# Kernel tuning notes

Hardware: AMD Instinct MI355X
Metric: run time of the kernel (lower is better)

## Reference

```python
import jax, jax.numpy as jnp
import numpy as np

NUM_NODES = 256
IN_FEAT = 64
HIDDEN = 512
N_CLASSES = 2
BATCH = 256


def setup_inputs() -> dict:
    key = jax.random.key(0)
    ks = jax.random.split(key, 10)
    return {
        "z": jax.random.normal(ks[0], (BATCH, 1, NUM_NODES, NUM_NODES), dtype=jnp.float32),
        "node_emb": jax.random.normal(ks[1], (NUM_NODES, IN_FEAT), dtype=jnp.float32),
        "w1": jax.random.normal(ks[2], (IN_FEAT, HIDDEN), dtype=jnp.float32) * (1.0 / np.sqrt(IN_FEAT)),
        "b1": jnp.zeros((HIDDEN,), dtype=jnp.float32),
        "w2": jax.random.normal(ks[3], (HIDDEN, HIDDEN), dtype=jnp.float32) * (1.0 / np.sqrt(HIDDEN)),
        "b2": jnp.zeros((HIDDEN,), dtype=jnp.float32),
        "w3": jax.random.normal(ks[4], (HIDDEN, HIDDEN), dtype=jnp.float32) * (1.0 / np.sqrt(HIDDEN)),
        "b3": jnp.zeros((HIDDEN,), dtype=jnp.float32),
        "fcw": jax.random.normal(ks[5], (HIDDEN, N_CLASSES), dtype=jnp.float32) * (1.0 / np.sqrt(HIDDEN)),
        "fcb": jnp.zeros((N_CLASSES,), dtype=jnp.float32),
    }


def reference(z, node_emb, w1, b1, w2, b2, w3, b3, fcw, fcb):
    # z: (B, 1, N, N) latent interpreted as weighted adjacency
    z_sq = jnp.squeeze(z, axis=1)                         # (B, N, N)
    A = jax.nn.sigmoid(z_sq)
    A = (A + jnp.swapaxes(A, 1, 2)) * 0.5                  # symmetrize
    A_hat = A + jnp.eye(A.shape[-1], dtype=A.dtype)[None]  # add self loops
    D_hat = jnp.sum(A_hat, axis=2) + 1e-6                  # (B, N) degrees
    d_inv_sqrt = D_hat ** -0.5
    # norm_A = D^{-1/2} A_hat D^{-1/2} via row/col scaling (same math as diag bmm)
    norm_A = A_hat * d_inv_sqrt[:, :, None] * d_inv_sqrt[:, None, :]

    X = jnp.broadcast_to(node_emb[None], (z.shape[0],) + node_emb.shape)  # (B, N, F)
    H1 = jax.nn.relu(jnp.einsum('bij,bjh->bih', norm_A, X @ w1 + b1))
    H2 = jax.nn.relu(jnp.einsum('bij,bjh->bih', norm_A, H1 @ w2 + b2))
    H3 = jax.nn.relu(jnp.einsum('bij,bjh->bih', norm_A, H2 @ w3 + b3))
    graph_emb = jnp.mean(H3, axis=1)                       # (B, H)
    logits = graph_emb @ fcw + fcb                         # (B, n_classes)
    return logits
```

## Files before the change

kernel.cpp:

```cpp
#include <hip/hip_runtime.h>
#include <stdint.h>

#define B_ 256
#define N_ 256
#define F_ 64
#define H_ 512

typedef _Float16 f16;
typedef _Float16 f16x8 __attribute__((ext_vector_type(8)));
typedef _Float16 f16x4 __attribute__((ext_vector_type(4)));
typedef float    f32x4 __attribute__((ext_vector_type(4)));

__device__ __forceinline__ float sigmoidf_(float x) {
    return 1.0f / (1.0f + __expf(-x));
}

__global__ __launch_bounds__(256) void k_pre(const float* __restrict__ z,
                                             const float* __restrict__ ne,
                                             const float* __restrict__ w1,
                                             const float* __restrict__ b1,
                                             const float* __restrict__ w2,
                                             const float* __restrict__ w3,
                                             f16* __restrict__ S,
                                             float* __restrict__ R,
                                             float* __restrict__ Cpart,
                                             f16* __restrict__ XW1t,
                                             f16* __restrict__ w2t,
                                             f16* __restrict__ w3t) {
    int bid = blockIdx.x;
    int tid = threadIdx.x;
    if (bid < 2048) {
        int b = bid >> 3, c = bid & 7;
        int lane = tid & 63, w = tid >> 6;
        float colacc[4] = {0.f, 0.f, 0.f, 0.f};
        for (int r = 0; r < 8; r++) {
            int i = c * 32 + w * 8 + r;
            size_t base = ((size_t)(b * N_ + i)) * N_;
            float4 v = *(const float4*)(z + base + lane * 4);
            float s0 = sigmoidf_(v.x), s1 = sigmoidf_(v.y),
                  s2 = sigmoidf_(v.z), s3 = sigmoidf_(v.w);
            f16x4 sv = { (f16)s0, (f16)s1, (f16)s2, (f16)s3 };
            *(f16x4*)(S + base + lane * 4) = sv;
            colacc[0] += s0; colacc[1] += s1; colacc[2] += s2; colacc[3] += s3;
            float rs = s0 + s1 + s2 + s3;
            for (int off = 32; off; off >>= 1) rs += __shfl_down(rs, off, 64);
            if (lane == 0) R[b * N_ + i] = rs;
        }
        __shared__ float cbuf[4][N_];
        #pragma unroll
        for (int k = 0; k < 4; k++) cbuf[w][lane * 4 + k] = colacc[k];
        __syncthreads();
        float s4 = cbuf[0][tid] + cbuf[1][tid] + cbuf[2][tid] + cbuf[3][tid];
        Cpart[((size_t)c * B_ + b) * N_ + tid] = s4;
    } else if (bid < 2560) {
        int h = bid - 2048, node = tid;
        float s = b1[h];
        #pragma unroll 8
        for (int k = 0; k < F_; k++) s += ne[node * F_ + k] * w1[k * H_ + h];
        XW1t[h * N_ + node] = (f16)s;
    } else {
        int idx4 = bid - 2560;
        int which = idx4 >> 10;
        const float* src = which ? w3 : w2;
        f16* dst = which ? w3t : w2t;
        int idx = (idx4 & 1023) * 256 + tid;
        int k = idx >> 9, n = idx & 511;
        dst[n * H_ + k] = (f16)src[k * H_ + n];
    }
}

__global__ __launch_bounds__(256) void k_norma3(const f16* __restrict__ S,
                                                const float* __restrict__ R,
                                                const float* __restrict__ Cpart,
                                                f16* __restrict__ nA) {
    __shared__ f16 T0[128 * 129];
    __shared__ f16 T1[128 * 129];
    __shared__ float Dv[N_];
    int b = blockIdx.y, t = blockIdx.x;
    int tid = threadIdx.x;
    const f16* Sb = S + (size_t)b * N_ * N_;
    f16* Ab = nA + (size_t)b * N_ * N_;

    float cs = 0.f;
    #pragma unroll
    for (int c = 0; c < 8; c++) cs += Cpart[((size_t)c * B_ + b) * N_ + tid];
    Dv[tid] = rsqrtf(1.0f + 1e-6f + 0.5f * (R[b * N_ + tid] + cs));

    auto stage = [&](const f16* src, f16* dst) {
        #pragma unroll
        for (int it = 0; it < 8; it++) {
            int u = it * 256 + tid;
            int r = u >> 4, c8 = (u & 15) * 8;
            *(f16x8*)&dst[r * 129 + c8] = *(const f16x8*)&src[(size_t)r * N_ + c8];
        }
    };
    if (t == 0)      stage(Sb, T0);
    else if (t == 1) stage(Sb + 128 * N_ + 128, T0);
    else           { stage(Sb + 128, T0); stage(Sb + (size_t)128 * N_, T1); }
    __syncthreads();

    auto emit = [&](const f16* Dir, const f16* Mir, int i0, int j0) {
        #pragma unroll
        for (int it = 0; it < 8; it++) {
            int il = it * 16 + (tid >> 4), jl8 = (tid & 15) * 8;
            float di = Dv[i0 + il];
            f16x8 d = *(const f16x8*)&Dir[il * 129 + jl8];
            f16x8 o;
            #pragma unroll
            for (int k = 0; k < 8; k++) {
                float v = 0.5f * ((float)d[k] + (float)Mir[(jl8 + k) * 129 + il]);
                if (i0 + il == j0 + jl8 + k) v += 1.0f;
                o[k] = (f16)(v * di * Dv[j0 + jl8 + k]);
            }
            *(f16x8*)&Ab[(size_t)(i0 + il) * N_ + j0 + jl8] = o;
        }
    };
    if (t == 0)      emit(T0, T0, 0, 0);
    else if (t == 1) emit(T0, T0, 128, 128);
    else           { emit(T0, T1, 0, 128); emit(T1, T0, 128, 0); }
}

template <int KDIM, int MODE>
__global__ __launch_bounds__(256, 4) void k_gemm(const f16* __restrict__ A, long aBatch,
                                                 const f16* __restrict__ Bt, long bBatch,
                                                 f16* __restrict__ Out,
                                                 const float* __restrict__ bias,
                                                 float* __restrict__ gp) {
    __shared__ f16 As[128 * 64];
    __shared__ f16 Bs[128 * 64];
    const int tid  = threadIdx.x;
    const int lane = tid & 63, wave = tid >> 6;
    const int wm = wave >> 1, wn = wave & 1;

    const int lin = blockIdx.x;
    const int xcd = lin & 7, q = lin >> 3;
    const int n_t = q & 3, p = q >> 2;
    const int grp = xcd * 64 + p;
    const int b   = grp >> 1, m_t = grp & 1;
    const int m0 = m_t * 128, n0 = n_t * 128;

    const f16* Ab = A + (size_t)b * aBatch;
    const f16* Bb = Bt + (size_t)b * bBatch;

    f32x4 acc[4][4];
    #pragma unroll
    for (int i = 0; i < 4; i++)
        #pragma unroll
        for (int j = 0; j < 4; j++)
            #pragma unroll
            for (int r = 0; r < 4; r++) acc[i][j][r] = 0.0f;

    const int lr = lane >> 3;
    const int kc = (lane & 7) ^ lr;

    const int ln15 = lane & 15;

    constexpr int NS = KDIM / 64;
    const int srot = ((q >> 5) + q) & (NS - 1);

    for (int si = 0; si < NS; si++) {
        const int kk = ((si + srot) & (NS - 1)) * 64;
        #pragma unroll
        for (int c = 0; c < 4; c++) {
            int chunk = wave * 4 + c;
            int row = chunk * 8 + lr;
            __builtin_amdgcn_global_load_lds(
                (__attribute__((address_space(1))) void*)(Ab + (size_t)(m0 + row) * KDIM + kk + kc * 8),
                (__attribute__((address_space(3))) void*)(&As[chunk * 512]), 16, 0, 0);
            __builtin_amdgcn_global_load_lds(
                (__attribute__((address_space(1))) void*)(Bb + (size_t)(n0 + row) * KDIM + kk + kc * 8),
                (__attribute__((address_space(3))) void*)(&Bs[chunk * 512]), 16, 0, 0);
        }
        __syncthreads();

        #pragma unroll
        for (int ks = 0; ks < 2; ks++) {
            const int rkc = ks * 4 + (lane >> 4);
            f16x8 aF[4];
            #pragma unroll
            for (int t = 0; t < 4; t++) {
                int ra = wm * 64 + t * 16 + ln15;
                aF[t] = *(const f16x8*)&As[(ra * 8 + (rkc ^ (ra & 7))) * 8];
            }
            #pragma unroll
            for (int h2 = 0; h2 < 2; h2++) {
                f16x8 bF[2];
                #pragma unroll
                for (int t = 0; t < 2; t++) {
                    int rb = wn * 64 + (h2 * 2 + t) * 16 + ln15;
                    bF[t] = *(const f16x8*)&Bs[(rb * 8 + (rkc ^ (rb & 7))) * 8];
                }
                #pragma unroll
                for (int mt = 0; mt < 4; mt++)
                    #pragma unroll
                    for (int t = 0; t < 2; t++)
                        acc[mt][h2 * 2 + t] = __builtin_amdgcn_mfma_f32_16x16x32_f16(aF[mt], bF[t], acc[mt][h2 * 2 + t], 0, 0, 0);
            }
        }
        __syncthreads();
    }

    const int quad = lane >> 4;
    if (MODE == 0) {
        f16* Ob = Out + (size_t)b * (N_ * H_);
        #pragma unroll
        for (int mt = 0; mt < 4; mt++) {
            int node = m0 + wm * 64 + mt * 16 + quad * 4;
            #pragma unroll
            for (int nt = 0; nt < 4; nt++) {
                int h = n0 + wn * 64 + nt * 16 + ln15;
                #pragma unroll
                for (int rr = 0; rr < 4; rr++) {
                    float v = acc[mt][nt][rr];
                    v = v > 0.f ? v : 0.f;
                    Ob[(size_t)(node + rr) * H_ + h] = (f16)v;
                }
            }
        }
    } else if (MODE == 1) {
        f16* Ob = Out + (size_t)b * (H_ * N_);
        #pragma unroll
        for (int nt = 0; nt < 4; nt++) {
            int n = n0 + wn * 64 + nt * 16 + ln15;
            float bv = bias[n];
            #pragma unroll
            for (int mt = 0; mt < 4; mt++) {
                int node = m0 + wm * 64 + mt * 16 + quad * 4;
                f16x4 v;
                #pragma unroll
                for (int rr = 0; rr < 4; rr++) v[rr] = (f16)(acc[mt][nt][rr] + bv);
                *(f16x4*)&Ob[(size_t)n * N_ + node] = v;
            }
        }
    } else {
        float part[4];
        #pragma unroll
        for (int nt = 0; nt < 4; nt++) {
            float partial = 0.f;
            #pragma unroll
            for (int mt = 0; mt < 4; mt++)
                #pragma unroll
                for (int rr = 0; rr < 4; rr++) {
                    float v = acc[mt][nt][rr];
                    partial += (v > 0.f ? v : 0.f);
                }
            partial += __shfl_down(partial, 32, 64);
            partial += __shfl_down(partial, 16, 64);
            part[nt] = partial;
        }
        __syncthreads();
        float* red = (float*)&As[0];
        if (quad == 0) {
            #pragma unroll
            for (int nt = 0; nt < 4; nt++)
                red[wave * 64 + nt * 16 + ln15] = part[nt];
        }
        __syncthreads();
        if (tid < 128) {
            int wnl = tid >> 6, hl = tid & 63;
            float v = red[wnl * 64 + hl] + red[(wnl + 2) * 64 + hl];
            gp[((size_t)m_t * B_ + b) * H_ + n0 + wnl * 64 + hl] = v;
        }
    }
}

__global__ __launch_bounds__(256) void k_logits(const float* __restrict__ gp,
                                                const float* __restrict__ fcw,
                                                const float* __restrict__ fcb,
                                                float* __restrict__ out) {
    int b = blockIdx.x, tid = threadIdx.x;
    const float* g0p = gp + (size_t)b * H_;
    const float* g1p = gp + (size_t)(B_ + b) * H_;
    float g0 = g0p[tid] + g1p[tid];
    float g1 = g0p[tid + 256] + g1p[tid + 256];
    float p0 = g0 * fcw[tid * 2 + 0] + g1 * fcw[(tid + 256) * 2 + 0];
    float p1 = g0 * fcw[tid * 2 + 1] + g1 * fcw[(tid + 256) * 2 + 1];
    for (int off = 32; off; off >>= 1) {
        p0 += __shfl_down(p0, off, 64);
        p1 += __shfl_down(p1, off, 64);
    }
    __shared__ float r0[4], r1[4];
    int lane = tid & 63, w = tid >> 6;
    if (lane == 0) { r0[w] = p0; r1[w] = p1; }
    __syncthreads();
    const float inv = 1.0f / N_;
    if (tid == 0) out[b * 2 + 0] = (r0[0] + r0[1] + r0[2] + r0[3]) * inv + fcb[0];
    if (tid == 1) out[b * 2 + 1] = (r1[0] + r1[1] + r1[2] + r1[3]) * inv + fcb[1];
}

extern "C" void kernel_launch(void* const* d_in, const int* in_sizes, int n_in,
                              void* d_out, int out_size, void* d_ws, size_t ws_size,
                              hipStream_t stream) {
    const float* z   = (const float*)d_in[0];
    const float* ne  = (const float*)d_in[1];
    const float* w1  = (const float*)d_in[2];
    const float* b1  = (const float*)d_in[3];
    const float* w2  = (const float*)d_in[4];
    const float* b2  = (const float*)d_in[5];
    const float* w3  = (const float*)d_in[6];
    const float* b3  = (const float*)d_in[7];
    const float* fcw = (const float*)d_in[8];
    const float* fcb = (const float*)d_in[9];
    float* out = (float*)d_out;

    char* ws = (char*)d_ws;
    f16*   T     = (f16*)(ws + 0);
    float* R     = (float*)(ws + 0);
    float* Cpart = (float*)(ws + 262144);
    f16*   nA    = (f16*)(ws + 67108864);
    f16*   Hh    = (f16*)(ws + 100663296);
    f16*   S     = (f16*)(ws + 100663296);
    float* gpart = (float*)(ws + 100663296);
    f16*   XW1t  = (f16*)(ws + 167772160);
    f16*   w2t   = (f16*)(ws + 168034304);
    f16*   w3t   = (f16*)(ws + 168558592);

    k_pre   <<<4608,        256, 0, stream>>>(z, ne, w1, b1, w2, w3, S, R, Cpart, XW1t, w2t, w3t);
    k_norma3<<<dim3(3, B_), 256, 0, stream>>>(S, R, Cpart, nA);

    k_gemm<256, 0><<<2048, 256, 0, stream>>>(nA, 65536, XW1t, 0, Hh, nullptr, nullptr);
    k_gemm<512, 1><<<2048, 256, 0, stream>>>(Hh, 131072, w2t, 0, T, b2, nullptr);
    k_gemm<256, 0><<<2048, 256, 0, stream>>>(nA, 65536, T, 131072, Hh, nullptr, nullptr);
    k_gemm<512, 1><<<2048, 256, 0, stream>>>(Hh, 131072, w3t, 0, T, b3, nullptr);
    k_gemm<256, 2><<<2048, 256, 0, stream>>>(nA, 65536, T, 131072, nullptr, nullptr, gpart);

    k_logits<<<B_, 256, 0, stream>>>(gpart, fcw, fcb, out);
}
```

Baseline: 335.4 us.

## Halve GEMM N-tile to 64, raise occupancy, fuse logits via atomics

Shrinks the GEMM output tile from 128x128 to 128x64, doubling the grid to 4096 blocks. This cuts accumulator registers and the B-tile LDS footprint so launch bounds can target 5 blocks per SM. It drops the K-stage rotation and fuses the final classifier into the last GEMM's epilogue with atomicAdd into a zeroed output, which removes the k_logits launch and the gpart round trip. In exchange the A tile is reloaded twice as often, and float atomics make the summation order nondeterministic.

```diff
diff --git a/kernel.cpp b/kernel.cpp
--- a/kernel.cpp
+++ b/kernel.cpp
@@ -121,45 +121,42 @@
 }
 
 template <int KDIM, int MODE>
-__global__ __launch_bounds__(256, 4) void k_gemm(const f16* __restrict__ A, long aBatch,
+__global__ __launch_bounds__(256, 5) void k_gemm(const f16* __restrict__ A, long aBatch,
                                                  const f16* __restrict__ Bt, long bBatch,
                                                  f16* __restrict__ Out,
                                                  const float* __restrict__ bias,
-                                                 float* __restrict__ gp) {
+                                                 const float* __restrict__ fcw,
+                                                 const float* __restrict__ fcb,
+                                                 float* __restrict__ logits) {
     __shared__ f16 As[128 * 64];
-    __shared__ f16 Bs[128 * 64];
+    __shared__ f16 Bs[64 * 64];
     const int tid  = threadIdx.x;
     const int lane = tid & 63, wave = tid >> 6;
     const int wm = wave >> 1, wn = wave & 1;
 
     const int lin = blockIdx.x;
     const int xcd = lin & 7, q = lin >> 3;
-    const int n_t = q & 3, p = q >> 2;
+    const int n_t = q & 7, p = q >> 3;
     const int grp = xcd * 64 + p;
     const int b   = grp >> 1, m_t = grp & 1;
-    const int m0 = m_t * 128, n0 = n_t * 128;
+    const int m0 = m_t * 128, n0 = n_t * 64;
 
     const f16* Ab = A + (size_t)b * aBatch;
     const f16* Bb = Bt + (size_t)b * bBatch;
 
-    f32x4 acc[4][4];
+    f32x4 acc[4][2];
     #pragma unroll
     for (int i = 0; i < 4; i++)
         #pragma unroll
-        for (int j = 0; j < 4; j++)
+        for (int j = 0; j < 2; j++)
             #pragma unroll
             for (int r = 0; r < 4; r++) acc[i][j][r] = 0.0f;
 
     const int lr = lane >> 3;
     const int kc = (lane & 7) ^ lr;
-
     const int ln15 = lane & 15;
 
-    constexpr int NS = KDIM / 64;
-    const int srot = ((q >> 5) + q) & (NS - 1);
-
-    for (int si = 0; si < NS; si++) {
-        const int kk = ((si + srot) & (NS - 1)) * 64;
+    for (int kk = 0; kk < KDIM; kk += 64) {
         #pragma unroll
         for (int c = 0; c < 4; c++) {
             int chunk = wave * 4 + c;
@@ -167,6 +164,11 @@
             __builtin_amdgcn_global_load_lds(
                 (__attribute__((address_space(1))) void*)(Ab + (size_t)(m0 + row) * KDIM + kk + kc * 8),
                 (__attribute__((address_space(3))) void*)(&As[chunk * 512]), 16, 0, 0);
+        }
+        #pragma unroll
+        for (int c = 0; c < 2; c++) {
+            int chunk = wave * 2 + c;
+            int row = chunk * 8 + lr;
             __builtin_amdgcn_global_load_lds(
                 (__attribute__((address_space(1))) void*)(Bb + (size_t)(n0 + row) * KDIM + kk + kc * 8),
                 (__attribute__((address_space(3))) void*)(&Bs[chunk * 512]), 16, 0, 0);
@@ -176,25 +178,19 @@
         #pragma unroll
         for (int ks = 0; ks < 2; ks++) {
             const int rkc = ks * 4 + (lane >> 4);
-            f16x8 aF[4];
-            #pragma unroll
-            for (int t = 0; t < 4; t++) {
-                int ra = wm * 64 + t * 16 + ln15;
-                aF[t] = *(const f16x8*)&As[(ra * 8 + (rkc ^ (ra & 7))) * 8];
-            }
-            #pragma unroll
-            for (int h2 = 0; h2 < 2; h2++) {
-                f16x8 bF[2];
+            f16x8 bF[2];
+            #pragma unroll
+            for (int t = 0; t < 2; t++) {
+                int rb = wn * 32 + t * 16 + ln15;
+                bF[t] = *(const f16x8*)&Bs[(rb * 8 + (rkc ^ (rb & 7))) * 8];
+            }
+            #pragma unroll
+            for (int mt = 0; mt < 4; mt++) {
+                int ra = wm * 64 + mt * 16 + ln15;
+                f16x8 aF = *(const f16x8*)&As[(ra * 8 + (rkc ^ (ra & 7))) * 8];
                 #pragma unroll
-                for (int t = 0; t < 2; t++) {
-                    int rb = wn * 64 + (h2 * 2 + t) * 16 + ln15;
-                    bF[t] = *(const f16x8*)&Bs[(rb * 8 + (rkc ^ (rb & 7))) * 8];
-                }
-                #pragma unroll
-                for (int mt = 0; mt < 4; mt++)
-                    #pragma unroll
-                    for (int t = 0; t < 2; t++)
-                        acc[mt][h2 * 2 + t] = __builtin_amdgcn_mfma_f32_16x16x32_f16(aF[mt], bF[t], acc[mt][h2 * 2 + t], 0, 0, 0);
+                for (int nt = 0; nt < 2; nt++)
+                    acc[mt][nt] = __builtin_amdgcn_mfma_f32_16x16x32_f16(aF, bF[nt], acc[mt][nt], 0, 0, 0);
             }
         }
         __syncthreads();
@@ -207,8 +203,8 @@
         for (int mt = 0; mt < 4; mt++) {
             int node = m0 + wm * 64 + mt * 16 + quad * 4;
             #pragma unroll
-            for (int nt = 0; nt < 4; nt++) {
-                int h = n0 + wn * 64 + nt * 16 + ln15;
+            for (int nt = 0; nt < 2; nt++) {
+                int h = n0 + wn * 32 + nt * 16 + ln15;
                 #pragma unroll
                 for (int rr = 0; rr < 4; rr++) {
                     float v = acc[mt][nt][rr];
@@ -220,8 +216,8 @@
     } else if (MODE == 1) {
         f16* Ob = Out + (size_t)b * (H_ * N_);
         #pragma unroll
-        for (int nt = 0; nt < 4; nt++) {
-            int n = n0 + wn * 64 + nt * 16 + ln15;
+        for (int nt = 0; nt < 2; nt++) {
+            int n = n0 + wn * 32 + nt * 16 + ln15;
             float bv = bias[n];
             #pragma unroll
             for (int mt = 0; mt < 4; mt++) {
@@ -233,9 +229,9 @@
             }
         }
     } else {
-        float part[4];
-        #pragma unroll
-        for (int nt = 0; nt < 4; nt++) {
+        float part[2];
+        #pragma unroll
+        for (int nt = 0; nt < 2; nt++) {
             float partial = 0.f;
             #pragma unroll
             for (int mt = 0; mt < 4; mt++)
@@ -252,40 +248,28 @@
         float* red = (float*)&As[0];
         if (quad == 0) {
             #pragma unroll
-            for (int nt = 0; nt < 4; nt++)
-                red[wave * 64 + nt * 16 + ln15] = part[nt];
-        }
-        __syncthreads();
-        if (tid < 128) {
-            int wnl = tid >> 6, hl = tid & 63;
-            float v = red[wnl * 64 + hl] + red[(wnl + 2) * 64 + hl];
-            gp[((size_t)m_t * B_ + b) * H_ + n0 + wnl * 64 + hl] = v;
-        }
+            for (int nt = 0; nt < 2; nt++)
+                red[wave * 32 + nt * 16 + ln15] = part[nt];
+        }
+        __syncthreads();
+        if (tid < 64) {
+            int wn2 = tid >> 5, x = tid & 31;
+            float g = red[wn2 * 32 + x] + red[(2 + wn2) * 32 + x];
+            int h = n0 + wn2 * 32 + x;
+            float p0 = g * fcw[h * 2 + 0];
+            float p1 = g * fcw[h * 2 + 1];
+            for (int off = 32; off; off >>= 1) {
+                p0 += __shfl_down(p0, off, 64);
+                p1 += __shfl_down(p1, off, 64);
+            }
+            if (tid == 0) {
+                atomicAdd(logits + b * 2 + 0, p0 * (1.0f / N_));
+                atomicAdd(logits + b * 2 + 1, p1 * (1.0f / N_));
+            }
+        }
+        if (m_t == 0 && n_t == 0 && tid < 2)
+            atomicAdd(logits + b * 2 + tid, fcb[tid]);
     }
-}
-
-__global__ __launch_bounds__(256) void k_logits(const float* __restrict__ gp,
-                                                const float* __restrict__ fcw,
-                                                const float* __restrict__ fcb,
-                                                float* __restrict__ out) {
-    int b = blockIdx.x, tid = threadIdx.x;
-    const float* g0p = gp + (size_t)b * H_;
-    const float* g1p = gp + (size_t)(B_ + b) * H_;
-    float g0 = g0p[tid] + g1p[tid];
-    float g1 = g0p[tid + 256] + g1p[tid + 256];
-    float p0 = g0 * fcw[tid * 2 + 0] + g1 * fcw[(tid + 256) * 2 + 0];
-    float p1 = g0 * fcw[tid * 2 + 1] + g1 * fcw[(tid + 256) * 2 + 1];
-    for (int off = 32; off; off >>= 1) {
-        p0 += __shfl_down(p0, off, 64);
-        p1 += __shfl_down(p1, off, 64);
-    }
-    __shared__ float r0[4], r1[4];
-    int lane = tid & 63, w = tid >> 6;
-    if (lane == 0) { r0[w] = p0; r1[w] = p1; }
-    __syncthreads();
-    const float inv = 1.0f / N_;
-    if (tid == 0) out[b * 2 + 0] = (r0[0] + r0[1] + r0[2] + r0[3]) * inv + fcb[0];
-    if (tid == 1) out[b * 2 + 1] = (r1[0] + r1[1] + r1[2] + r1[3]) * inv + fcb[1];
 }
 
 extern "C" void kernel_launch(void* const* d_in, const int* in_sizes, int n_in,
@@ -310,7 +294,6 @@
     f16*   nA    = (f16*)(ws + 67108864);
     f16*   Hh    = (f16*)(ws + 100663296);
     f16*   S     = (f16*)(ws + 100663296);
-    float* gpart = (float*)(ws + 100663296);
     f16*   XW1t  = (f16*)(ws + 167772160);
     f16*   w2t   = (f16*)(ws + 168034304);
     f16*   w3t   = (f16*)(ws + 168558592);
@@ -318,11 +301,10 @@
     k_pre   <<<4608,        256, 0, stream>>>(z, ne, w1, b1, w2, w3, S, R, Cpart, XW1t, w2t, w3t);
     k_norma3<<<dim3(3, B_), 256, 0, stream>>>(S, R, Cpart, nA);
 
-    k_gemm<256, 0><<<2048, 256, 0, stream>>>(nA, 65536, XW1t, 0, Hh, nullptr, nullptr);
-    k_gemm<512, 1><<<2048, 256, 0, stream>>>(Hh, 131072, w2t, 0, T, b2, nullptr);
-    k_gemm<256, 0><<<2048, 256, 0, stream>>>(nA, 65536, T, 131072, Hh, nullptr, nullptr);
-    k_gemm<512, 1><<<2048, 256, 0, stream>>>(Hh, 131072, w3t, 0, T, b3, nullptr);
-    k_gemm<256, 2><<<2048, 256, 0, stream>>>(nA, 65536, T, 131072, nullptr, nullptr, gpart);
-
-    k_logits<<<B_, 256, 0, stream>>>(gpart, fcw, fcb, out);
-}
+    k_gemm<256, 0><<<4096, 256, 0, stream>>>(nA, 65536, XW1t, 0, Hh, nullptr, nullptr, nullptr, nullptr);
+    k_gemm<512, 1><<<4096, 256, 0, stream>>>(Hh, 131072, w2t, 0, T, b2, nullptr, nullptr, nullptr);
+    k_gemm<256, 0><<<4096, 256, 0, stream>>>(nA, 65536, T, 131072, Hh, nullptr, nullptr, nullptr, nullptr);
+    k_gemm<512, 1><<<4096, 256, 0, stream>>>(Hh, 131072, w3t, 0, T, b3, nullptr, nullptr, nullptr);
+    hipMemsetAsync(out, 0, (size_t)out_size * sizeof(float), stream);
+    k_gemm<256, 2><<<4096, 256, 0, stream>>>(nA, 65536, T, 131072, nullptr, nullptr, fcw, fcb, out);
+}
```

Result: slower. 349.6 us (+4.2%).

## Load shared weights directly to registers and fuse logits into final GEMM

Applied to the files above, without the earlier changes.

For the two weight GEMMs (Hh×w2t, Hh×w3t), the B operand is now read from global memory straight into double-buffered registers instead of being staged through LDS. Occupancy is lowered to 3 blocks to make room for these registers. The final aggregation GEMM now computes the classifier logits itself, using warp reductions and atomicAdd into a zeroed output, which removes the separate logits kernel and the gpart round trip. The k-loop stagger rotation is also dropped, so concurrent blocks may hit the same rows at once, and the atomic accumulation makes the logits order-nondeterministic.

```diff
diff --git a/kernel.cpp b/kernel.cpp
--- a/kernel.cpp
+++ b/kernel.cpp
@@ -120,14 +120,17 @@
     else           { emit(T0, T1, 0, 128); emit(T1, T0, 128, 0); }
 }
 
-template <int KDIM, int MODE>
-__global__ __launch_bounds__(256, 4) void k_gemm(const f16* __restrict__ A, long aBatch,
-                                                 const f16* __restrict__ Bt, long bBatch,
-                                                 f16* __restrict__ Out,
-                                                 const float* __restrict__ bias,
-                                                 float* __restrict__ gp) {
+template <int KDIM, int MODE, int BDIR>
+__global__ __launch_bounds__(256, BDIR ? 3 : 4) void k_gemm(
+        const f16* __restrict__ A, long aBatch,
+        const f16* __restrict__ Bt, long bBatch,
+        f16* __restrict__ Out,
+        const float* __restrict__ bias,
+        const float* __restrict__ fcw,
+        const float* __restrict__ fcb,
+        float* __restrict__ logits) {
     __shared__ f16 As[128 * 64];
-    __shared__ f16 Bs[128 * 64];
+    __shared__ f16 Bs[BDIR ? 64 : 128 * 64];
     const int tid  = threadIdx.x;
     const int lane = tid & 63, wave = tid >> 6;
     const int wm = wave >> 1, wn = wave & 1;
@@ -152,14 +155,23 @@
 
     const int lr = lane >> 3;
     const int kc = (lane & 7) ^ lr;
-
-    const int ln15 = lane & 15;
+    const int ln15 = lane & 15, quad = lane >> 4;
+
+    f16x8 bB[2][8];
+    const f16* pBbase = Bb + (size_t)(n0 + wn * 64 + ln15) * KDIM + quad * 8;
+    auto loadB = [&](int buf, int kk) {
+        #pragma unroll
+        for (int ks = 0; ks < 2; ks++)
+            #pragma unroll
+            for (int t = 0; t < 4; t++)
+                bB[buf][ks * 4 + t] = *(const f16x8*)(pBbase + (size_t)t * 16 * KDIM + kk + ks * 32);
+    };
+
+    if (BDIR) loadB(0, 0);
 
     constexpr int NS = KDIM / 64;
-    const int srot = ((q >> 5) + q) & (NS - 1);
-
-    for (int si = 0; si < NS; si++) {
-        const int kk = ((si + srot) & (NS - 1)) * 64;
+    for (int s = 0; s < NS; s++) {
+        const int kk = s * 64;
         #pragma unroll
         for (int c = 0; c < 4; c++) {
             int chunk = wave * 4 + c;
@@ -167,40 +179,50 @@
             __builtin_amdgcn_global_load_lds(
                 (__attribute__((address_space(1))) void*)(Ab + (size_t)(m0 + row) * KDIM + kk + kc * 8),
                 (__attribute__((address_space(3))) void*)(&As[chunk * 512]), 16, 0, 0);
-            __builtin_amdgcn_global_load_lds(
-                (__attribute__((address_space(1))) void*)(Bb + (size_t)(n0 + row) * KDIM + kk + kc * 8),
-                (__attribute__((address_space(3))) void*)(&Bs[chunk * 512]), 16, 0, 0);
+            if (!BDIR)
+                __builtin_amdgcn_global_load_lds(
+                    (__attribute__((address_space(1))) void*)(Bb + (size_t)(n0 + row) * KDIM + kk + kc * 8),
+                    (__attribute__((address_space(3))) void*)(&Bs[BDIR ? 0 : chunk * 512]), 16, 0, 0);
         }
         __syncthreads();
 
+        if (BDIR && s + 1 < NS) loadB((s + 1) & 1, kk + 64);
+
         #pragma unroll
         for (int ks = 0; ks < 2; ks++) {
-            const int rkc = ks * 4 + (lane >> 4);
+            const int rkc = ks * 4 + quad;
             f16x8 aF[4];
             #pragma unroll
             for (int t = 0; t < 4; t++) {
                 int ra = wm * 64 + t * 16 + ln15;
                 aF[t] = *(const f16x8*)&As[(ra * 8 + (rkc ^ (ra & 7))) * 8];
             }
-            #pragma unroll
-            for (int h2 = 0; h2 < 2; h2++) {
-                f16x8 bF[2];
-                #pragma unroll
-                for (int t = 0; t < 2; t++) {
-                    int rb = wn * 64 + (h2 * 2 + t) * 16 + ln15;
-                    bF[t] = *(const f16x8*)&Bs[(rb * 8 + (rkc ^ (rb & 7))) * 8];
-                }
+            if (BDIR) {
                 #pragma unroll
                 for (int mt = 0; mt < 4; mt++)
                     #pragma unroll
-                    for (int t = 0; t < 2; t++)
-                        acc[mt][h2 * 2 + t] = __builtin_amdgcn_mfma_f32_16x16x32_f16(aF[mt], bF[t], acc[mt][h2 * 2 + t], 0, 0, 0);
+                    for (int nt = 0; nt < 4; nt++)
+                        acc[mt][nt] = __builtin_amdgcn_mfma_f32_16x16x32_f16(aF[mt], bB[s & 1][ks * 4 + nt], acc[mt][nt], 0, 0, 0);
+            } else {
+                #pragma unroll
+                for (int h2 = 0; h2 < 2; h2++) {
+                    f16x8 bF[2];
+                    #pragma unroll
+                    for (int t = 0; t < 2; t++) {
+                        int rb = wn * 64 + (h2 * 2 + t) * 16 + ln15;
+                        bF[t] = *(const f16x8*)&Bs[BDIR ? 0 : (rb * 8 + (rkc ^ (rb & 7))) * 8];
+                    }
+                    #pragma unroll
+                    for (int mt = 0; mt < 4; mt++)
+                        #pragma unroll
+                        for (int t = 0; t < 2; t++)
+                            acc[mt][h2 * 2 + t] = __builtin_amdgcn_mfma_f32_16x16x32_f16(aF[mt], bF[t], acc[mt][h2 * 2 + t], 0, 0, 0);
+                }
             }
         }
         __syncthreads();
     }
 
-    const int quad = lane >> 4;
     if (MODE == 0) {
         f16* Ob = Out + (size_t)b * (N_ * H_);
         #pragma unroll
@@ -248,7 +270,6 @@
             partial += __shfl_down(partial, 16, 64);
             part[nt] = partial;
         }
-        __syncthreads();
         float* red = (float*)&As[0];
         if (quad == 0) {
             #pragma unroll
@@ -257,35 +278,23 @@
         }
         __syncthreads();
         if (tid < 128) {
-            int wnl = tid >> 6, hl = tid & 63;
-            float v = red[wnl * 64 + hl] + red[(wnl + 2) * 64 + hl];
-            gp[((size_t)m_t * B_ + b) * H_ + n0 + wnl * 64 + hl] = v;
-        }
+            int w2 = tid >> 6, x = tid & 63;
+            float g = red[w2 * 64 + x] + red[(w2 + 2) * 64 + x];
+            int h = n0 + w2 * 64 + x;
+            float p0 = g * fcw[h * 2 + 0];
+            float p1 = g * fcw[h * 2 + 1];
+            for (int off = 32; off; off >>= 1) {
+                p0 += __shfl_down(p0, off, 64);
+                p1 += __shfl_down(p1, off, 64);
+            }
+            if ((tid & 63) == 0) {
+                atomicAdd(logits + b * 2 + 0, p0 * (1.0f / N_));
+                atomicAdd(logits + b * 2 + 1, p1 * (1.0f / N_));
+            }
+        }
+        if (m_t == 0 && n_t == 0 && tid < 2)
+            atomicAdd(logits + b * 2 + tid, fcb[tid]);
     }
-}
-
-__global__ __launch_bounds__(256) void k_logits(const float* __restrict__ gp,
-                                                const float* __restrict__ fcw,
-                                                const float* __restrict__ fcb,
-                                                float* __restrict__ out) {
-    int b = blockIdx.x, tid = threadIdx.x;
-    const float* g0p = gp + (size_t)b * H_;
-    const float* g1p = gp + (size_t)(B_ + b) * H_;
-    float g0 = g0p[tid] + g1p[tid];
-    float g1 = g0p[tid + 256] + g1p[tid + 256];
-    float p0 = g0 * fcw[tid * 2 + 0] + g1 * fcw[(tid + 256) * 2 + 0];
-    float p1 = g0 * fcw[tid * 2 + 1] + g1 * fcw[(tid + 256) * 2 + 1];
-    for (int off = 32; off; off >>= 1) {
-        p0 += __shfl_down(p0, off, 64);
-        p1 += __shfl_down(p1, off, 64);
-    }
-    __shared__ float r0[4], r1[4];
-    int lane = tid & 63, w = tid >> 6;
-    if (lane == 0) { r0[w] = p0; r1[w] = p1; }
-    __syncthreads();
-    const float inv = 1.0f / N_;
-    if (tid == 0) out[b * 2 + 0] = (r0[0] + r0[1] + r0[2] + r0[3]) * inv + fcb[0];
-    if (tid == 1) out[b * 2 + 1] = (r1[0] + r1[1] + r1[2] + r1[3]) * inv + fcb[1];
 }
 
 extern "C" void kernel_launch(void* const* d_in, const int* in_sizes, int n_in,
@@ -310,7 +319,6 @@
     f16*   nA    = (f16*)(ws + 67108864);
     f16*   Hh    = (f16*)(ws + 100663296);
     f16*   S     = (f16*)(ws + 100663296);
-    float* gpart = (float*)(ws + 100663296);
     f16*   XW1t  = (f16*)(ws + 167772160);
     f16*   w2t   = (f16*)(ws + 168034304);
     f16*   w3t   = (f16*)(ws + 168558592);
@@ -318,11 +326,10 @@
     k_pre   <<<4608,        256, 0, stream>>>(z, ne, w1, b1, w2, w3, S, R, Cpart, XW1t, w2t, w3t);
     k_norma3<<<dim3(3, B_), 256, 0, stream>>>(S, R, Cpart, nA);
 
-    k_gemm<256, 0><<<2048, 256, 0, stream>>>(nA, 65536, XW1t, 0, Hh, nullptr, nullptr);
-    k_gemm<512, 1><<<2048, 256, 0, stream>>>(Hh, 131072, w2t, 0, T, b2, nullptr);
-    k_gemm<256, 0><<<2048, 256, 0, stream>>>(nA, 65536, T, 131072, Hh, nullptr, nullptr);
-    k_gemm<512, 1><<<2048, 256, 0, stream>>>(Hh, 131072, w3t, 0, T, b3, nullptr);
-    k_gemm<256, 2><<<2048, 256, 0, stream>>>(nA, 65536, T, 131072, nullptr, nullptr, gpart);
-
-    k_logits<<<B_, 256, 0, stream>>>(gpart, fcw, fcb, out);
-}
+    k_gemm<256, 0, 0><<<2048, 256, 0, stream>>>(nA, 65536, XW1t, 0, Hh, nullptr, nullptr, nullptr, nullptr);
+    k_gemm<512, 1, 1><<<2048, 256, 0, stream>>>(Hh, 131072, w2t, 0, T, b2, nullptr, nullptr, nullptr);
+    k_gemm<256, 0, 0><<<2048, 256, 0, stream>>>(nA, 65536, T, 131072, Hh, nullptr, nullptr, nullptr, nullptr);
+    k_gemm<512, 1, 1><<<2048, 256, 0, stream>>>(Hh, 131072, w3t, 0, T, b3, nullptr, nullptr, nullptr);
+    hipMemsetAsync(out, 0, (size_t)out_size * sizeof(float), stream);
+    k_gemm<256, 2, 0><<<2048, 256, 0, stream>>>(nA, 65536, T, 131072, nullptr, nullptr, fcw, fcb, out);
+}
```

After: 435.1 us. 1.3x slower.
